# Kernel optimization log

Hardware: AMD Instinct MI355X
Metric: run time of the kernel (lower is better)

Reference implementation:

```python
import jax, jax.numpy as jnp
import numpy as np

B, P, C, F, E = 8, 65536, 32768, 32, 524288  # batch, n_paths, n_channels, feature, edges


def setup_inputs() -> dict:
    key = jax.random.key(0)
    ks = jax.random.split(key, 8)
    path_features = jax.random.normal(ks[0], (B, P, F), jnp.float32)
    channel_features = jax.random.normal(ks[1], (B, C, F), jnp.float32)
    edge_path = jax.random.randint(ks[2], (E,), 0, P)
    edge_channel = jnp.sort(jax.random.randint(ks[3], (E,), 0, C))
    s = 1.0 / np.sqrt(F)  # PyTorch GRU default init range
    W_ih = jax.random.uniform(ks[4], (3 * F, F), jnp.float32, -s, s)
    W_hh = jax.random.uniform(ks[5], (3 * F, F), jnp.float32, -s, s)
    b_ih = jax.random.uniform(ks[6], (3 * F,), jnp.float32, -s, s)
    b_hh = jax.random.uniform(ks[7], (3 * F,), jnp.float32, -s, s)
    return dict(path_features=path_features, channel_features=channel_features,
                W_ih=W_ih, W_hh=W_hh, b_ih=b_ih, b_hh=b_hh,
                edge_path=edge_path, edge_channel=edge_channel)


def reference(path_features, channel_features, W_ih, W_hh, b_ih, b_hh, edge_path, edge_channel):
    # Ragged per-channel sum of path features (segment-sum over edge list)
    gathered = jnp.swapaxes(path_features[:, edge_path, :], 0, 1)          # [E, B, F]
    agg = jax.ops.segment_sum(gathered, edge_channel, num_segments=C)      # [C, B, F]
    x = jnp.swapaxes(agg, 0, 1)                                            # [B, C, F]
    h = channel_features                                                   # [B, C, F]
    # Single-step GRU (PyTorch gate order: r, z, n)
    gx = x @ W_ih.T + b_ih                                                 # [B, C, 3F]
    gh = h @ W_hh.T + b_hh
    xr, xz, xn = jnp.split(gx, 3, axis=-1)
    hr, hz, hn = jnp.split(gh, 3, axis=-1)
    r = jax.nn.sigmoid(xr + hr)
    z = jax.nn.sigmoid(xz + hz)
    n = jnp.tanh(xn + r * hn)
    return (1.0 - z) * n + z * h                                           # [B, C, F]
```

## Files before the change

kernel.cpp:

```cpp
#include <hip/hip_runtime.h>
#include <hip/hip_fp16.h>

#define NB 8
#define NP 65536
#define NC 32768
#define NF 32
#define NE 524288
#define XROW 40
#define CHB 64
#define CAP 2048
#define CONV_BLOCKS 8192

typedef __attribute__((ext_vector_type(4))) float floatx4;
typedef __attribute__((ext_vector_type(8))) short short8;
typedef __attribute__((ext_vector_type(4))) short short4v;

struct h4 { __half2 lo, hi; };
struct h8 { __half2 a, b, c, d; };

__device__ __forceinline__ floatx4 h4tof4(h4 v) {
    float2 a = __half22float2(v.lo);
    float2 b = __half22float2(v.hi);
    floatx4 r; r[0] = a.x; r[1] = a.y; r[2] = b.x; r[3] = b.y;
    return r;
}

__device__ __forceinline__ short f2b(float f) {
    union { float f; unsigned int u; } v;
    v.f = f;
    unsigned int lsb = (v.u >> 16) & 1u;
    v.u += 0x7fffu + lsb;
    return (short)(v.u >> 16);
}

__device__ __forceinline__ int lower_bound(const int* __restrict__ a, int v) {
    int lo = 0, hi = NE;
    while (lo < hi) {
        int mid = (lo + hi) >> 1;
        if (a[mid] < v) lo = mid + 1; else hi = mid;
    }
    return lo;
}

__device__ __forceinline__ float sigmoidf_(float v) {
    return 1.f / (1.f + __expf(-v));
}
__device__ __forceinline__ float tanhf_(float v) {
    v = fminf(v, 40.f);
    float t = __expf(2.f * v);
    return (t - 1.f) / (t + 1.f);
}

__global__ __launch_bounds__(256) void prep_kernel(
    const float* __restrict__ path, __half* __restrict__ pathH,
    const int* __restrict__ edge_channel, int* __restrict__ bounds)
{
    if (blockIdx.x < CONV_BLOCKS) {
        const size_t id = ((size_t)blockIdx.x * 256 + threadIdx.x) * 8;
        floatx4 v0 = __builtin_nontemporal_load((const floatx4*)(path + id));
        floatx4 v1 = __builtin_nontemporal_load((const floatx4*)(path + id + 4));
        h8 o;
        o.a = __floats2half2_rn(v0[0], v0[1]);
        o.b = __floats2half2_rn(v0[2], v0[3]);
        o.c = __floats2half2_rn(v1[0], v1[1]);
        o.d = __floats2half2_rn(v1[2], v1[3]);
        union { h8 s; floatx4 f; } cv; cv.s = o;
        __builtin_nontemporal_store(cv.f, (floatx4*)(pathH + id));
    } else {
        const int c = (blockIdx.x - CONV_BLOCKS) * 256 + threadIdx.x;
        if (c <= NC) bounds[c] = lower_bound(edge_channel, c);
    }
}

__global__ __launch_bounds__(256) void fused_gru_new(
    const __half* __restrict__ pathH,
    const float*  __restrict__ hbuf,
    const float*  __restrict__ W_ih,
    const float*  __restrict__ W_hh,
    const float*  __restrict__ b_ih,
    const float*  __restrict__ b_hh,
    const int*    __restrict__ edge_path,
    const int*    __restrict__ bounds,
    float*        __restrict__ out)
{
    const int t    = threadIdx.x;
    const int w    = t >> 6;
    const int lane = t & 63;
    const int batch = blockIdx.x & 7;
    const int c0    = (blockIdx.x >> 3) * CHB;

    __shared__ __align__(16) short xs [64 * XROW];
    __shared__ __align__(16) short wsx[96 * XROW];
    __shared__ __align__(16) short wsh[96 * XROW];
    __shared__ int lbnd[CHB + 1];
    __shared__ int eidx[CAP];

    for (int idx = t; idx < 96 * NF; idx += 256) {
        int r = idx >> 5, c = idx & 31;
        wsx[r * XROW + c] = f2b(W_ih[idx]);
        wsh[r * XROW + c] = f2b(W_hh[idx]);
    }
    if (t <= CHB) lbnd[t] = bounds[c0 + t];

    const int base = bounds[c0];
    const int cnt  = bounds[c0 + CHB] - base;
    const int cntc = cnt < CAP ? cnt : CAP;
    for (int j = t; j < cntc; j += 256) eidx[j] = edge_path[base + j];
    __syncthreads();

    const int g  = t >> 2;
    const int fh = t & 3;
    const __half* pbase = pathH + (size_t)batch * (NP * NF) + fh * 8;

    const int ls = lbnd[g];
    const int le = lbnd[g + 1];
    floatx4 accL = {0.f, 0.f, 0.f, 0.f};
    floatx4 accH = {0.f, 0.f, 0.f, 0.f};

    auto run_gather = [&](auto IDX) {
        for (int i = ls; i < le; i += 8) {
            int i1 = i + 1, i2 = i + 2, i3 = i + 3;
            int i4 = i + 4, i5 = i + 5, i6 = i + 6, i7 = i + 7;
            int p0 = IDX(i);
            int p1 = IDX(i1 < le ? i1 : i);
            int p2 = IDX(i2 < le ? i2 : i);
            int p3 = IDX(i3 < le ? i3 : i);
            int p4 = IDX(i4 < le ? i4 : i);
            int p5 = IDX(i5 < le ? i5 : i);
            int p6 = IDX(i6 < le ? i6 : i);
            int p7 = IDX(i7 < le ? i7 : i);
            h8 g0 = *(const h8*)(pbase + (size_t)p0 * NF);
            h8 g1 = *(const h8*)(pbase + (size_t)p1 * NF);
            h8 g2 = *(const h8*)(pbase + (size_t)p2 * NF);
            h8 g3 = *(const h8*)(pbase + (size_t)p3 * NF);
            h8 g4 = *(const h8*)(pbase + (size_t)p4 * NF);
            h8 g5 = *(const h8*)(pbase + (size_t)p5 * NF);
            h8 g6 = *(const h8*)(pbase + (size_t)p6 * NF);
            h8 g7 = *(const h8*)(pbase + (size_t)p7 * NF);
            h4 a0; a0.lo = g0.a; a0.hi = g0.b;  h4 b0; b0.lo = g0.c; b0.hi = g0.d;
            accL += h4tof4(a0); accH += h4tof4(b0);
            if (i1 < le) { h4 a; a.lo = g1.a; a.hi = g1.b; h4 b; b.lo = g1.c; b.hi = g1.d;
                           accL += h4tof4(a); accH += h4tof4(b); }
            if (i2 < le) { h4 a; a.lo = g2.a; a.hi = g2.b; h4 b; b.lo = g2.c; b.hi = g2.d;
                           accL += h4tof4(a); accH += h4tof4(b); }
            if (i3 < le) { h4 a; a.lo = g3.a; a.hi = g3.b; h4 b; b.lo = g3.c; b.hi = g3.d;
                           accL += h4tof4(a); accH += h4tof4(b); }
            if (i4 < le) { h4 a; a.lo = g4.a; a.hi = g4.b; h4 b; b.lo = g4.c; b.hi = g4.d;
                           accL += h4tof4(a); accH += h4tof4(b); }
            if (i5 < le) { h4 a; a.lo = g5.a; a.hi = g5.b; h4 b; b.lo = g5.c; b.hi = g5.d;
                           accL += h4tof4(a); accH += h4tof4(b); }
            if (i6 < le) { h4 a; a.lo = g6.a; a.hi = g6.b; h4 b; b.lo = g6.c; b.hi = g6.d;
                           accL += h4tof4(a); accH += h4tof4(b); }
            if (i7 < le) { h4 a; a.lo = g7.a; a.hi = g7.b; h4 b; b.lo = g7.c; b.hi = g7.d;
                           accL += h4tof4(a); accH += h4tof4(b); }
        }
    };

    if (cnt <= CAP) {
        run_gather([&](int j) { return eidx[j - base]; });
    } else {
        run_gather([&](int j) { return edge_path[j]; });
    }

    {
        short8 xb;
        #pragma unroll
        for (int q = 0; q < 4; ++q) { xb[q] = f2b(accL[q]); xb[4 + q] = f2b(accH[q]); }
        *(short8*)(&xs[g * XROW + fh * 8]) = xb;
    }
    __syncthreads();

    const int quad = lane >> 4;
    const int n16  = lane & 15;
    const int k0   = quad * 8;

    const int rA = w * 16 + n16;
    short8 ax = *(const short8*)(&xs[rA * XROW + k0]);

    const size_t mrow = (size_t)batch * NC + c0;
    const float* hrow = hbuf + (mrow + rA) * NF + k0;
    floatx4 h0 = __builtin_nontemporal_load((const floatx4*)(hrow));
    floatx4 h1 = __builtin_nontemporal_load((const floatx4*)(hrow + 4));
    short8 ah;
    #pragma unroll
    for (int q = 0; q < 4; ++q) { ah[q] = f2b(h0[q]); ah[4 + q] = f2b(h1[q]); }

    float bxv[6], bhv[6];
    #pragma unroll
    for (int tt = 0; tt < 6; ++tt) {
        bxv[tt] = b_ih[16 * tt + n16];
        bhv[tt] = b_hh[16 * tt + n16];
    }

    const floatx4 zero = {0.f, 0.f, 0.f, 0.f};
    floatx4 gg[4];
    #pragma unroll
    for (int tt = 0; tt < 4; ++tt) {
        short8 bw = *(const short8*)(&wsx[(16 * tt + n16) * XROW + k0]);
        floatx4 a = __builtin_amdgcn_mfma_f32_16x16x32_bf16(ax, bw, zero, 0, 0, 0);
        bw = *(const short8*)(&wsh[(16 * tt + n16) * XROW + k0]);
        gg[tt] = __builtin_amdgcn_mfma_f32_16x16x32_bf16(ah, bw, a, 0, 0, 0);
    }
    floatx4 nx[2], nh[2];
    #pragma unroll
    for (int u = 0; u < 2; ++u) {
        const int tt = 4 + u;
        short8 bw = *(const short8*)(&wsx[(16 * tt + n16) * XROW + k0]);
        nx[u] = __builtin_amdgcn_mfma_f32_16x16x32_bf16(ax, bw, zero, 0, 0, 0);
        bw = *(const short8*)(&wsh[(16 * tt + n16) * XROW + k0]);
        nh[u] = __builtin_amdgcn_mfma_f32_16x16x32_bf16(ah, bw, zero, 0, 0, 0);
    }

    #pragma unroll
    for (int i = 0; i < 4; ++i) {
        const int r2 = w * 16 + quad * 4 + i;
        const size_t m = mrow + r2;
        float r0 = sigmoidf_(gg[0][i] + bxv[0] + bhv[0]);
        float r1 = sigmoidf_(gg[1][i] + bxv[1] + bhv[1]);
        float z0 = sigmoidf_(gg[2][i] + bxv[2] + bhv[2]);
        float z1 = sigmoidf_(gg[3][i] + bxv[3] + bhv[3]);
        float n0 = tanhf_(nx[0][i] + bxv[4] + r0 * (nh[0][i] + bhv[4]));
        float n1 = tanhf_(nx[1][i] + bxv[5] + r1 * (nh[1][i] + bhv[5]));
        float hv0 = __builtin_nontemporal_load(&hbuf[m * NF + n16]);
        float hv1 = __builtin_nontemporal_load(&hbuf[m * NF + 16 + n16]);
        __builtin_nontemporal_store((1.f - z0) * n0 + z0 * hv0, &out[m * NF + n16]);
        __builtin_nontemporal_store((1.f - z1) * n1 + z1 * hv1, &out[m * NF + 16 + n16]);
    }
}

__global__ __launch_bounds__(256) void fused_gru_fb(
    const float*  __restrict__ path,
    const float*  __restrict__ hbuf,
    const float*  __restrict__ W_ih,
    const float*  __restrict__ W_hh,
    const float*  __restrict__ b_ih,
    const float*  __restrict__ b_hh,
    const int*    __restrict__ edge_path,
    const int*    __restrict__ edge_channel,
    float*        __restrict__ out)
{
    const int t    = threadIdx.x;
    const int w    = t >> 6;
    const int lane = t & 63;
    const int cblk = blockIdx.x * 8;

    __shared__ int bounds[9];
    __shared__ __align__(16) short xs [64 * XROW];
    __shared__ __align__(16) short wsx[96 * XROW];
    __shared__ __align__(16) short wsh[96 * XROW];

    if (t < 9) bounds[t] = lower_bound(edge_channel, cblk + t);
    for (int idx = t; idx < 96 * NF; idx += 256) {
        int r = idx >> 5, c = idx & 31;
        wsx[r * XROW + c] = f2b(W_ih[idx]);
        wsh[r * XROW + c] = f2b(W_hh[idx]);
    }
    __syncthreads();

    const int b  = lane >> 3;
    const int fq = lane & 7;
    const float* prow = path + (size_t)b * (NP * NF) + fq * 4;

    #pragma unroll
    for (int half = 0; half < 2; ++half) {
        const int cl = w * 2 + half;
        const int s = __builtin_amdgcn_readfirstlane(bounds[cl]);
        const int e = __builtin_amdgcn_readfirstlane(bounds[cl + 1]);
        floatx4 acc = {0.f, 0.f, 0.f, 0.f};
        int i = s;
        for (; i + 8 <= e; i += 8) {
            int p0 = edge_path[i + 0], p1 = edge_path[i + 1];
            int p2 = edge_path[i + 2], p3 = edge_path[i + 3];
            int p4 = edge_path[i + 4], p5 = edge_path[i + 5];
            int p6 = edge_path[i + 6], p7 = edge_path[i + 7];
            floatx4 g0 = *(const floatx4*)(prow + (size_t)p0 * NF);
            floatx4 g1 = *(const floatx4*)(prow + (size_t)p1 * NF);
            floatx4 g2 = *(const floatx4*)(prow + (size_t)p2 * NF);
            floatx4 g3 = *(const floatx4*)(prow + (size_t)p3 * NF);
            floatx4 g4 = *(const floatx4*)(prow + (size_t)p4 * NF);
            floatx4 g5 = *(const floatx4*)(prow + (size_t)p5 * NF);
            floatx4 g6 = *(const floatx4*)(prow + (size_t)p6 * NF);
            floatx4 g7 = *(const floatx4*)(prow + (size_t)p7 * NF);
            acc += ((g0 + g1) + (g2 + g3)) + ((g4 + g5) + (g6 + g7));
        }
        for (; i < e; ++i)
            acc += *(const floatx4*)(prow + (size_t)edge_path[i] * NF);
        short4v xb;
        #pragma unroll
        for (int q = 0; q < 4; ++q) xb[q] = f2b(acc[q]);
        *(short4v*)(&xs[(b * 8 + cl) * XROW + fq * 4]) = xb;
    }
    __syncthreads();

    const int quad = lane >> 4;
    const int n16  = lane & 15;
    const int k0   = quad * 8;

    const int rA = w * 16 + n16;
    short8 ax = *(const short8*)(&xs[rA * XROW + k0]);
    const int bA = rA >> 3;
    const int cA = cblk + (rA & 7);
    const float* hrow = hbuf + ((size_t)bA * NC + cA) * NF + k0;
    floatx4 h0 = *(const floatx4*)(hrow);
    floatx4 h1 = *(const floatx4*)(hrow + 4);
    short8 ah;
    #pragma unroll
    for (int q = 0; q < 4; ++q) { ah[q] = f2b(h0[q]); ah[4 + q] = f2b(h1[q]); }

    float bxv[6], bhv[6];
    #pragma unroll
    for (int tt = 0; tt < 6; ++tt) {
        bxv[tt] = b_ih[16 * tt + n16];
        bhv[tt] = b_hh[16 * tt + n16];
    }
    const floatx4 zero = {0.f, 0.f, 0.f, 0.f};
    floatx4 g[4];
    #pragma unroll
    for (int tt = 0; tt < 4; ++tt) {
        short8 bw = *(const short8*)(&wsx[(16 * tt + n16) * XROW + k0]);
        floatx4 a = __builtin_amdgcn_mfma_f32_16x16x32_bf16(ax, bw, zero, 0, 0, 0);
        bw = *(const short8*)(&wsh[(16 * tt + n16) * XROW + k0]);
        g[tt] = __builtin_amdgcn_mfma_f32_16x16x32_bf16(ah, bw, a, 0, 0, 0);
    }
    floatx4 nx[2], nh[2];
    #pragma unroll
    for (int u = 0; u < 2; ++u) {
        const int tt = 4 + u;
        short8 bw = *(const short8*)(&wsx[(16 * tt + n16) * XROW + k0]);
        nx[u] = __builtin_amdgcn_mfma_f32_16x16x32_bf16(ax, bw, zero, 0, 0, 0);
        bw = *(const short8*)(&wsh[(16 * tt + n16) * XROW + k0]);
        nh[u] = __builtin_amdgcn_mfma_f32_16x16x32_bf16(ah, bw, zero, 0, 0, 0);
    }
    #pragma unroll
    for (int i = 0; i < 4; ++i) {
        const int r  = w * 16 + quad * 4 + i;
        const int b2 = r >> 3;
        const size_t m = (size_t)b2 * NC + (cblk + (r & 7));
        float r0 = sigmoidf_(g[0][i] + bxv[0] + bhv[0]);
        float r1 = sigmoidf_(g[1][i] + bxv[1] + bhv[1]);
        float z0 = sigmoidf_(g[2][i] + bxv[2] + bhv[2]);
        float z1 = sigmoidf_(g[3][i] + bxv[3] + bhv[3]);
        float n0 = tanhf_(nx[0][i] + bxv[4] + r0 * (nh[0][i] + bhv[4]));
        float n1 = tanhf_(nx[1][i] + bxv[5] + r1 * (nh[1][i] + bhv[5]));
        float hv0 = hbuf[m * NF + n16];
        float hv1 = hbuf[m * NF + 16 + n16];
        out[m * NF + n16]      = (1.f - z0) * n0 + z0 * hv0;
        out[m * NF + 16 + n16] = (1.f - z1) * n1 + z1 * hv1;
    }
}

extern "C" void kernel_launch(void* const* d_in, const int* in_sizes, int n_in,
                              void* d_out, int out_size, void* d_ws, size_t ws_size,
                              hipStream_t stream) {
    const float* path = (const float*)d_in[0];
    const float* chan = (const float*)d_in[1];
    const float* W_ih = (const float*)d_in[2];
    const float* W_hh = (const float*)d_in[3];
    const float* b_ih = (const float*)d_in[4];
    const float* b_hh = (const float*)d_in[5];
    const int* edge_path    = (const int*)d_in[6];
    const int* edge_channel = (const int*)d_in[7];
    float* out = (float*)d_out;

    const size_t pathH_bytes = (size_t)NB * NP * NF * sizeof(__half);
    const size_t need = pathH_bytes + (size_t)(NC + 1) * sizeof(int);
    if (ws_size >= need) {
        __half* pathH = (__half*)d_ws;
        int* bounds = (int*)((char*)d_ws + pathH_bytes);
        const int bblocks = (NC + 1 + 255) / 256;
        prep_kernel<<<dim3(CONV_BLOCKS + bblocks), dim3(256), 0, stream>>>(
            path, pathH, edge_channel, bounds);
        fused_gru_new<<<dim3((NC / CHB) * NB), dim3(256), 0, stream>>>(
            pathH, chan, W_ih, W_hh, b_ih, b_hh, edge_path, bounds, out);
    } else {
        fused_gru_fb<<<dim3(NC / 8), dim3(256), 0, stream>>>(
            path, chan, W_ih, W_hh, b_ih, b_hh, edge_path, edge_channel, out);
    }
}
```

Measured before the change: 210.2 us.

## Double channels per block, pre-convert GRU weights once, store edge indices as 16-bit

The fused GRU kernel now handles 128 channels per block with 512 threads, and the edge-index staging capacity doubles. The fp32-to-bf16 weight conversion moves out of every block into one extra block of the prep kernel; each fused block then copies the ready bf16 weights into shared memory with vector loads. Staged edge indices are stored as 16-bit values, since path indices fit under 65536, which halves the shared-memory footprint. This cuts repeated weight conversion and per-block setup, at the cost of fewer, larger blocks and possible changes to occupancy and load balance.

Result: faster. 194.8 us (-7.3%).

```diff
diff --git a/kernel.cpp b/kernel.cpp
--- a/kernel.cpp
+++ b/kernel.cpp
@@ -7,8 +7,8 @@
 #define NF 32
 #define NE 524288
 #define XROW 40
-#define CHB 64
-#define CAP 2048
+#define CHB 128
+#define CAP 4096
 #define CONV_BLOCKS 8192
 
 typedef __attribute__((ext_vector_type(4))) float floatx4;
@@ -53,8 +53,11 @@
 
 __global__ __launch_bounds__(256) void prep_kernel(
     const float* __restrict__ path, __half* __restrict__ pathH,
-    const int* __restrict__ edge_channel, int* __restrict__ bounds)
+    const int* __restrict__ edge_channel, int* __restrict__ bounds,
+    const float* __restrict__ W_ih, const float* __restrict__ W_hh,
+    unsigned short* __restrict__ wb)
 {
+    const int bblocks = (NC + 1 + 255) / 256;
     if (blockIdx.x < CONV_BLOCKS) {
         const size_t id = ((size_t)blockIdx.x * 256 + threadIdx.x) * 8;
         floatx4 v0 = __builtin_nontemporal_load((const floatx4*)(path + id));
@@ -66,17 +69,21 @@
         o.d = __floats2half2_rn(v1[2], v1[3]);
         union { h8 s; floatx4 f; } cv; cv.s = o;
         __builtin_nontemporal_store(cv.f, (floatx4*)(pathH + id));
-    } else {
+    } else if (blockIdx.x < CONV_BLOCKS + bblocks) {
         const int c = (blockIdx.x - CONV_BLOCKS) * 256 + threadIdx.x;
         if (c <= NC) bounds[c] = lower_bound(edge_channel, c);
-    }
-}
-
-__global__ __launch_bounds__(256) void fused_gru_new(
+    } else {
+        for (int j = threadIdx.x; j < 96 * NF; j += 256) {
+            wb[j]           = (unsigned short)f2b(W_ih[j]);
+            wb[96 * NF + j] = (unsigned short)f2b(W_hh[j]);
+        }
+    }
+}
+
+__global__ __launch_bounds__(512) void fused_gru_new(
     const __half* __restrict__ pathH,
     const float*  __restrict__ hbuf,
-    const float*  __restrict__ W_ih,
-    const float*  __restrict__ W_hh,
+    const unsigned short* __restrict__ wb,
     const float*  __restrict__ b_ih,
     const float*  __restrict__ b_hh,
     const int*    __restrict__ edge_path,
@@ -89,23 +96,27 @@
     const int batch = blockIdx.x & 7;
     const int c0    = (blockIdx.x >> 3) * CHB;
 
-    __shared__ __align__(16) short xs [64 * XROW];
+    __shared__ __align__(16) short xs [CHB * XROW];
     __shared__ __align__(16) short wsx[96 * XROW];
     __shared__ __align__(16) short wsh[96 * XROW];
     __shared__ int lbnd[CHB + 1];
-    __shared__ int eidx[CAP];
-
-    for (int idx = t; idx < 96 * NF; idx += 256) {
-        int r = idx >> 5, c = idx & 31;
-        wsx[r * XROW + c] = f2b(W_ih[idx]);
-        wsh[r * XROW + c] = f2b(W_hh[idx]);
+    __shared__ unsigned short eidx[CAP];
+
+    {
+        const int j = t;
+        if (j < 384) {
+            const int r = j >> 2, c = (j & 3) * 8;
+            *(short8*)(&wsx[r * XROW + c]) = *(const short8*)(&wb[r * NF + c]);
+            *(short8*)(&wsh[r * XROW + c]) = *(const short8*)(&wb[96 * NF + r * NF + c]);
+        }
     }
     if (t <= CHB) lbnd[t] = bounds[c0 + t];
 
     const int base = bounds[c0];
     const int cnt  = bounds[c0 + CHB] - base;
     const int cntc = cnt < CAP ? cnt : CAP;
-    for (int j = t; j < cntc; j += 256) eidx[j] = edge_path[base + j];
+    for (int j = t; j < cntc; j += 512)
+        eidx[j] = (unsigned short)edge_path[base + j];
     __syncthreads();
 
     const int g  = t >> 2;
@@ -157,7 +168,7 @@
     };
 
     if (cnt <= CAP) {
-        run_gather([&](int j) { return eidx[j - base]; });
+        run_gather([&](int j) { return (int)eidx[j - base]; });
     } else {
         run_gather([&](int j) { return edge_path[j]; });
     }
@@ -363,15 +374,18 @@
     float* out = (float*)d_out;
 
     const size_t pathH_bytes = (size_t)NB * NP * NF * sizeof(__half);
-    const size_t need = pathH_bytes + (size_t)(NC + 1) * sizeof(int);
+    const size_t bounds_bytes = (size_t)(NC + 1) * sizeof(int);
+    const size_t wb_bytes = (size_t)2 * 96 * NF * sizeof(unsigned short);
+    const size_t need = pathH_bytes + bounds_bytes + wb_bytes;
     if (ws_size >= need) {
         __half* pathH = (__half*)d_ws;
         int* bounds = (int*)((char*)d_ws + pathH_bytes);
+        unsigned short* wb = (unsigned short*)((char*)d_ws + pathH_bytes + bounds_bytes);
         const int bblocks = (NC + 1 + 255) / 256;
-        prep_kernel<<<dim3(CONV_BLOCKS + bblocks), dim3(256), 0, stream>>>(
-            path, pathH, edge_channel, bounds);
-        fused_gru_new<<<dim3((NC / CHB) * NB), dim3(256), 0, stream>>>(
-            pathH, chan, W_ih, W_hh, b_ih, b_hh, edge_path, bounds, out);
+        prep_kernel<<<dim3(CONV_BLOCKS + bblocks + 1), dim3(256), 0, stream>>>(
+            path, pathH, edge_channel, bounds, W_ih, W_hh, wb);
+        fused_gru_new<<<dim3((NC / CHB) * NB), dim3(512), 0, stream>>>(
+            pathH, chan, wb, b_ih, b_hh, edge_path, bounds, out);
     } else {
         fused_gru_fb<<<dim3(NC / 8), dim3(256), 0, stream>>>(
             path, chan, W_ih, W_hh, b_ih, b_hh, edge_path, edge_channel, out);
```
